# Kernel tuning notes

Measured on AMD Instinct MI355X. Metric: run time of the kernel, lower is better.

Reference implementation:

```python
import jax, jax.numpy as jnp
import numpy as np

N = 100_000      # nodes
E = 1_600_000    # edges (avg degree 16)
H = 2            # heads
C = 32           # out channels per head
L = 4            # EGAT layers
IN = 4           # input one-hot dim (node labels)
ECLS = 5         # edge classes (ratings)
SCALE = 0.1


def setup_inputs() -> dict:
    key = jax.random.key(0)
    ks = jax.random.split(key, 8)
    # node labels arange%4 -> equal user (0) / item (1) counts; x is one-hot (input_embedding=False)
    labels = jnp.arange(N) % 4
    x = jax.nn.one_hot(labels, IN, dtype=jnp.float32)
    edge_index = jax.random.randint(ks[0], (2, E), 0, N)
    edge_attr = jax.random.randint(ks[1], (E,), 0, ECLS)
    W0 = jax.random.normal(ks[2], (IN, H * C), dtype=jnp.float32) * SCALE
    W13 = jax.random.normal(ks[3], (L - 1, H * C, H * C), dtype=jnp.float32) * SCALE
    eemb = jax.random.normal(ks[4], (L, ECLS, H * C), dtype=jnp.float32) * SCALE
    att_src = jax.random.normal(ks[5], (L, H, C), dtype=jnp.float32) * SCALE
    att_dst = jax.random.normal(ks[6], (L, H, C), dtype=jnp.float32) * SCALE
    bias = jnp.zeros((L, H * C), dtype=jnp.float32)
    return dict(x=x, W0=W0, W13=W13, eemb=eemb, att_src=att_src,
                att_dst=att_dst, bias=bias, edge_index=edge_index, edge_attr=edge_attr)


def _egat_layer(x, W, eemb_l, a_src, a_dst, b, src, dst, edge_attr):
    # x: [N, Fin] -> h: [N, H, C]
    h = (x @ W).reshape(N, H, C)
    e = eemb_l[edge_attr].reshape(E, H, C)            # per-edge type embedding
    m = h[src] + e                                    # [E, H, C] edge-featured message
    logits = jax.nn.leaky_relu(
        jnp.sum(h[dst] * a_dst, axis=-1) + jnp.sum(m * a_src, axis=-1), 0.2)  # [E, H]
    # ragged softmax over incoming edges of each destination node
    amax = jax.ops.segment_max(logits, dst, num_segments=N)
    amax = jnp.where(jnp.isfinite(amax), amax, 0.0)
    ex = jnp.exp(logits - amax[dst])
    denom = jax.ops.segment_sum(ex, dst, num_segments=N)
    alpha = ex / (denom[dst] + 1e-16)                 # [E, H]
    out = jax.ops.segment_sum(alpha[..., None] * m, dst, num_segments=N)  # [N, H, C]
    return jax.nn.elu(out.reshape(N, H * C) + b)      # concat heads + elu activation


def reference(x, W0, W13, eemb, att_src, att_dst, bias, edge_index, edge_attr):
    src, dst = edge_index[0], edge_index[1]
    h = _egat_layer(x, W0, eemb[0], att_src[0], att_dst[0], bias[0], src, dst, edge_attr)
    for l in range(1, L):
        h = _egat_layer(h, W13[l - 1], eemb[l], att_src[l], att_dst[l], bias[l], src, dst, edge_attr)
    # users are nodes with label 0 (x[:,0]==1), items label 1 (x[:,1]==1);
    # labels were built as arange(N)%4, so user/item indices are static strided slices.
    user_idx = jnp.arange(0, N, 4)
    item_idx = jnp.arange(1, N, 4)
    u = h[user_idx]
    v = h[item_idx]
    return jnp.sum(u * v, axis=-1)  # MF decoder, multiply_by=1
```

## Files before the change

kernel.cpp:

```cpp
#include <hip/hip_runtime.h>
#include <hip/hip_bf16.h>
#include <math.h>

#define N_NODES 100000
#define N_EDGES 1600000
#define HC 64
#define NHEADS 2
#define NLAYERS 4
#define ECLS 5
#define NBUCK 196
#define NBLK 256
#define EPB (N_EDGES / NBLK)
#define NGRP (N_NODES / 16)
#define LIN0_BLOCKS 1024

typedef __attribute__((ext_vector_type(8))) short short8;
typedef __attribute__((ext_vector_type(4))) float floatx4;
union F8 { uint4 u; short8 s; };

__device__ inline float bf_lo(unsigned int u) { return __uint_as_float(u << 16); }
__device__ inline float bf_hi(unsigned int u) { return __uint_as_float(u & 0xffff0000u); }
__device__ inline unsigned short f2bf(float f) {
    unsigned int u = __float_as_uint(f);
    u += 0x7FFFu + ((u >> 16) & 1u);
    return (unsigned short)(u >> 16);
}

__global__ void k_chist_lin0(const int* __restrict__ dst, int* __restrict__ bh,
                             const float* __restrict__ in,
                             const float* __restrict__ W,
                             const float* __restrict__ asrc, const float* __restrict__ adst,
                             unsigned short* __restrict__ hcurb,
                             float* __restrict__ ssrc, float* __restrict__ sdst) {
    int tid = threadIdx.x;
    if (blockIdx.x < NBLK) {
        __shared__ int lh[NBUCK];
        int blk = blockIdx.x;
        for (int i = tid; i < NBUCK; i += 256) lh[i] = 0;
        __syncthreads();
        int s = blk * EPB, e = s + EPB;
        for (int i = s + tid; i < e; i += 256) atomicAdd(&lh[dst[i] >> 9], 1);
        __syncthreads();
        for (int i = tid; i < NBUCK; i += 256) bh[i * 256 + blk] = lh[i];
        return;
    }
    int j = tid & 63;
    int wid = ((blockIdx.x - NBLK) * 256 + tid) >> 6;
    int nwaves = LIN0_BLOCKS * 4;

    float w0 = W[0 * HC + j], w1 = W[1 * HC + j], w2 = W[2 * HC + j], w3 = W[3 * HC + j];
    int head = j >> 5;
    int c = j & 31;
    float as = asrc[head * 32 + c];
    float ad = adst[head * 32 + c];

    for (int n = wid; n < N_NODES; n += nwaves) {
        int nu = __builtin_amdgcn_readfirstlane(n);
        float4 r = *(const float4*)(in + (size_t)nu * 4);
        float acc = r.x * w0 + r.y * w1 + r.z * w2 + r.w * w3;
        hcurb[(size_t)nu * HC + j] = f2bf(acc);
        float ps = acc * as;
        float pd = acc * ad;
        for (int off = 16; off > 0; off >>= 1) {
            ps += __shfl_down(ps, off, 32);
            pd += __shfl_down(pd, off, 32);
        }
        if (c == 0) {
            ssrc[nu * 2 + head] = ps;
            sdst[nu * 2 + head] = pd;
        }
    }
}

__global__ void k_s1(const int* __restrict__ bh, int* __restrict__ bbase,
                     int* __restrict__ part) {
    __shared__ int tmp[256];
    int tid = threadIdx.x;
    int i = blockIdx.x * 256 + tid;
    int v = bh[i];
    tmp[tid] = v;
    __syncthreads();
    for (int off = 1; off < 256; off <<= 1) {
        int t = (tid >= off) ? tmp[tid - off] : 0;
        __syncthreads();
        tmp[tid] += t;
        __syncthreads();
    }
    bbase[i] = tmp[tid] - v;
    if (tid == 255) part[blockIdx.x] = tmp[255];
}

__global__ void k_s2(int* __restrict__ part,
                     const float* __restrict__ eemb, const float* __restrict__ att_src,
                     float* __restrict__ escore) {
    __shared__ int tmp[256];
    int tid = threadIdx.x;
    int v = (tid < NBUCK) ? part[tid] : 0;
    tmp[tid] = v;
    __syncthreads();
    for (int off = 1; off < 256; off <<= 1) {
        int t = (tid >= off) ? tmp[tid - off] : 0;
        __syncthreads();
        tmp[tid] += t;
        __syncthreads();
    }
    if (tid < NBUCK) part[tid] = tmp[tid] - v;
    if (tid >= 200 && tid < 200 + NLAYERS * ECLS * NHEADS) {
        int idx = tid - 200;
        int l = idx / (ECLS * NHEADS);
        int r = idx % (ECLS * NHEADS);
        int c = r >> 1;
        int h = r & 1;
        float s = 0.f;
        const float* ev = eemb + l * ECLS * HC + c * HC + h * 32;
        const float* av = att_src + l * HC + h * 32;
        for (int k = 0; k < 32; ++k) s += ev[k] * av[k];
        escore[idx] = s;
    }
}

__global__ void k_cscatter(const int* __restrict__ src, const int* __restrict__ dst,
                           const int* __restrict__ attr, const int* __restrict__ bbase,
                           const int* __restrict__ part, int* __restrict__ bkt) {
    __shared__ int cur[NBUCK];
    int tid = threadIdx.x, blk = blockIdx.x;
    for (int i = tid; i < NBUCK; i += 256) cur[i] = bbase[i * 256 + blk] + part[i];
    __syncthreads();
    int s0 = blk * EPB, e0 = s0 + EPB;
    for (int i = s0 + tid; i < e0; i += 256) {
        int d = dst[i];
        int b = d >> 9;
        int pos = atomicAdd(&cur[b], 1);
        bkt[pos] = src[i] | (attr[i] << 17) | ((d & 511) << 20);
    }
}

__global__ void k_fine(const int* __restrict__ part, const int* __restrict__ bkt,
                       int* __restrict__ packed, int* __restrict__ rowstart) {
    __shared__ int hist[512];
    __shared__ int cur[512];
    int b = blockIdx.x, tid = threadIdx.x;
    int base = part[b];
    int bend = (b + 1 < NBUCK) ? part[b + 1] : N_EDGES;
    int nb = bend - base;
    hist[tid] = 0;
    __syncthreads();
    for (int i = tid; i < nb; i += 512)
        atomicAdd(&hist[(bkt[base + i] >> 20) & 0x1FF], 1);
    __syncthreads();
    int v = hist[tid];
    for (int off = 1; off < 512; off <<= 1) {
        int t = (tid >= off) ? hist[tid - off] : 0;
        __syncthreads();
        hist[tid] += t;
        __syncthreads();
    }
    int excl = hist[tid] - v;
    int node = (b << 9) + tid;
    if (node <= N_NODES) rowstart[node] = base + excl;
    cur[tid] = excl;
    __syncthreads();
    for (int i = tid; i < nb; i += 512) {
        int p = bkt[base + i];
        int r = atomicAdd(&cur[(p >> 20) & 0x1FF], 1);
        packed[base + r] = p;
    }
}

__global__ void k_linmfma(const unsigned short* __restrict__ actB,
                          const float* __restrict__ Wl,
                          const float* __restrict__ asrc,
                          const float* __restrict__ adst,
                          unsigned short* __restrict__ hcurb,
                          float* __restrict__ ssrc, float* __restrict__ sdst) {
    __shared__ uint4 WB[512];
    __shared__ unsigned short Cb[4][1024];
    int tid = threadIdx.x;
    int lane = tid & 63;
    int w = tid >> 6;
    int q = lane >> 4;
    int c = lane & 15;

    for (int rid = tid; rid < 512; rid += 256) {
        int kk = rid >> 8;
        int t  = (rid >> 6) & 3;
        int ln = rid & 63;
        int qq = ln >> 4, cc = ln & 15;
        unsigned int u[4];
        #pragma unroll
        for (int jj = 0; jj < 4; ++jj) {
            float v0 = Wl[(kk * 32 + qq * 8 + jj * 2 + 0) * 64 + 16 * t + cc];
            float v1 = Wl[(kk * 32 + qq * 8 + jj * 2 + 1) * 64 + 16 * t + cc];
            u[jj] = (unsigned int)f2bf(v0) | ((unsigned int)f2bf(v1) << 16);
        }
        WB[rid] = make_uint4(u[0], u[1], u[2], u[3]);
    }
    __syncthreads();

    short8 bfr[2][4];
    #pragma unroll
    for (int kk = 0; kk < 2; ++kk)
        #pragma unroll
        for (int t = 0; t < 4; ++t) {
            F8 tmp; tmp.u = WB[(kk * 4 + t) * 64 + lane];
            bfr[kk][t] = tmp.s;
        }

    float as_[4], ad_[4];
    #pragma unroll
    for (int t = 0; t < 4; ++t) {
        as_[t] = asrc[16 * t + c];
        ad_[t] = adst[16 * t + c];
    }

    int wid = (blockIdx.x * 256 + tid) >> 6;
    int nwaves = gridDim.x * 4;

    for (int g = wid; g < NGRP; g += nwaves) {
        int base = g * 16;
        F8 a0, a1;
        a0.u = *(const uint4*)(actB + (size_t)(base + c) * HC + q * 8);
        a1.u = *(const uint4*)(actB + (size_t)(base + c) * HC + 32 + q * 8);

        floatx4 acc[4];
        #pragma unroll
        for (int t = 0; t < 4; ++t) {
            acc[t] = (floatx4){0.f, 0.f, 0.f, 0.f};
            acc[t] = __builtin_amdgcn_mfma_f32_16x16x32_bf16(a0.s, bfr[0][t], acc[t], 0, 0, 0);
            acc[t] = __builtin_amdgcn_mfma_f32_16x16x32_bf16(a1.s, bfr[1][t], acc[t], 0, 0, 0);
        }

        #pragma unroll
        for (int r = 0; r < 4; ++r) {
            float h0s = acc[0][r] * as_[0] + acc[1][r] * as_[1];
            float h1s = acc[2][r] * as_[2] + acc[3][r] * as_[3];
            float h0d = acc[0][r] * ad_[0] + acc[1][r] * ad_[1];
            float h1d = acc[2][r] * ad_[2] + acc[3][r] * ad_[3];
            #pragma unroll
            for (int off = 1; off < 16; off <<= 1) {
                h0s += __shfl_xor(h0s, off, 64);
                h1s += __shfl_xor(h1s, off, 64);
                h0d += __shfl_xor(h0d, off, 64);
                h1d += __shfl_xor(h1d, off, 64);
            }
            if (c == 0) {
                int node = base + q * 4 + r;
                *(float2*)(ssrc + node * 2) = make_float2(h0s, h1s);
                *(float2*)(sdst + node * 2) = make_float2(h0d, h1d);
            }
        }

        #pragma unroll
        for (int t = 0; t < 4; ++t)
            #pragma unroll
            for (int r = 0; r < 4; ++r)
                Cb[w][(q * 4 + r) * 64 + 16 * t + c] = f2bf(acc[t][r]);
        __builtin_amdgcn_wave_barrier();
        const uint4* cf = (const uint4*)&Cb[w][0];
        uint4* gout = (uint4*)(hcurb + (size_t)base * HC);
        gout[lane] = cf[lane];
        gout[64 + lane] = cf[64 + lane];
        __builtin_amdgcn_wave_barrier();
    }
}

template <int NW, bool LAST>
__global__ void k_edge(const int* __restrict__ rowstart, const int* __restrict__ packed,
                       const float* __restrict__ ssrc, const float* __restrict__ sdst,
                       const float* __restrict__ escore_l,
                       const unsigned short* __restrict__ hcurb,
                       const float* __restrict__ eemb_l,
                       const float* __restrict__ bias_l,
                       unsigned short* __restrict__ actnext, float* __restrict__ out) {
    __shared__ float lbuf[NW][64];
    __shared__ float obuf[2][64];
    int w = threadIdx.x >> 6;
    int n = LAST ? (blockIdx.x * 4 + w) : (blockIdx.x * NW + w);
    int lane = threadIdx.x & 63;
    int sub = lane >> 3;
    int q   = lane & 7;
    int h   = q >> 2;

    int beg = rowstart[n];
    int end = rowstart[n + 1];
    float sd = sdst[n * 2 + h];

    float4 a0 = make_float4(0.f, 0.f, 0.f, 0.f);
    float4 a1 = make_float4(0.f, 0.f, 0.f, 0.f);
    float ssum = 0.f;
    for (int i = beg + sub; i < end; i += 8) {
        int p = packed[i];
        int s = p & 0x1FFFF;
        int a = (p >> 17) & 7;
        float lg = sd + ssrc[s * 2 + h] + escore_l[a * 2 + h];
        lg = lg >= 0.f ? lg : 0.2f * lg;
        float wt = __expf(lg);
        uint4 hv = *(const uint4*)(hcurb + (size_t)s * HC + q * 8);
        const float4* ep = (const float4*)(eemb_l + a * HC + q * 8);
        float4 e0 = ep[0], e1 = ep[1];
        a0.x += wt * (bf_lo(hv.x) + e0.x);
        a0.y += wt * (bf_hi(hv.x) + e0.y);
        a0.z += wt * (bf_lo(hv.y) + e0.z);
        a0.w += wt * (bf_hi(hv.y) + e0.w);
        a1.x += wt * (bf_lo(hv.z) + e1.x);
        a1.y += wt * (bf_hi(hv.z) + e1.y);
        a1.z += wt * (bf_lo(hv.w) + e1.z);
        a1.w += wt * (bf_hi(hv.w) + e1.w);
        ssum += wt;
    }
    for (int off = 8; off < 64; off <<= 1) {
        a0.x += __shfl_xor(a0.x, off, 64);
        a0.y += __shfl_xor(a0.y, off, 64);
        a0.z += __shfl_xor(a0.z, off, 64);
        a0.w += __shfl_xor(a0.w, off, 64);
        a1.x += __shfl_xor(a1.x, off, 64);
        a1.y += __shfl_xor(a1.y, off, 64);
        a1.z += __shfl_xor(a1.z, off, 64);
        a1.w += __shfl_xor(a1.w, off, 64);
        ssum  += __shfl_xor(ssum,  off, 64);
    }
    if (sub == 0) {
        ((float4*)&lbuf[w][q * 8])[0] = a0;
        ((float4*)&lbuf[w][q * 8])[1] = a1;
    }
    float ssum_h = __shfl(ssum, (lane >> 5) * 4, 64);
    float inv = 1.f / (ssum_h + 1e-16f);
    __builtin_amdgcn_wave_barrier();
    float v = lbuf[w][lane] * inv + bias_l[lane];
    float o = v > 0.f ? v : (__expf(v) - 1.f);
    if (!LAST) {
        actnext[(size_t)n * HC + lane] = f2bf(o);
    } else {
        obuf[w][lane] = o;
        __syncthreads();
        if (w == 0) {
            float p = obuf[0][lane] * obuf[1][lane];
            for (int off = 32; off > 0; off >>= 1) p += __shfl_down(p, off, 64);
            if (lane == 0) out[blockIdx.x] = p;
        }
    }
}

extern "C" void kernel_launch(void* const* d_in, const int* in_sizes, int n_in,
                              void* d_out, int out_size, void* d_ws, size_t ws_size,
                              hipStream_t stream) {
    const float* x       = (const float*)d_in[0];
    const float* W0      = (const float*)d_in[1];
    const float* W13     = (const float*)d_in[2];
    const float* eemb    = (const float*)d_in[3];
    const float* att_src = (const float*)d_in[4];
    const float* att_dst = (const float*)d_in[5];
    const float* bias    = (const float*)d_in[6];
    const int*   eidx    = (const int*)d_in[7];
    const int*   eattr   = (const int*)d_in[8];
    float* out = (float*)d_out;

    const int* src = eidx;
    const int* dst = eidx + N_EDGES;

    char* wsb = (char*)d_ws;
    size_t off = 0;
    auto alloc = [&](size_t bytes) { char* p = wsb + off; off += (bytes + 255) & ~(size_t)255; return p; };
    unsigned short* hcurb  = (unsigned short*)alloc((size_t)N_NODES * HC * 2);
    unsigned short* actB   = (unsigned short*)alloc((size_t)N_NODES * HC * 2);
    float*          ssrc   = (float*)alloc((size_t)N_NODES * 2 * 4);
    float*          sdst   = (float*)alloc((size_t)N_NODES * 2 * 4);
    float*          escore = (float*)alloc(NLAYERS * ECLS * NHEADS * 4);
    int*            bh     = (int*)alloc((size_t)NBUCK * 256 * 4);
    int*            bbase  = (int*)alloc((size_t)NBUCK * 256 * 4);
    int*            part   = (int*)alloc(256 * 4);
    int*            rowstart = (int*)alloc(((size_t)N_NODES + 1) * 4);
    int*            bkt    = (int*)alloc((size_t)N_EDGES * 4);
    int*            packed = (int*)alloc((size_t)N_EDGES * 4);

    k_chist_lin0<<<NBLK + LIN0_BLOCKS, 256, 0, stream>>>(
        dst, bh, x, W0, att_src, att_dst, hcurb, ssrc, sdst);
    k_s1<<<NBUCK, 256, 0, stream>>>(bh, bbase, part);
    k_s2<<<1, 256, 0, stream>>>(part, eemb, att_src, escore);
    k_cscatter<<<NBLK, 256, 0, stream>>>(src, dst, eattr, bbase, part, bkt);
    k_fine<<<NBUCK, 512, 0, stream>>>(part, bkt, packed, rowstart);

    for (int l = 0; l < NLAYERS; ++l) {
        if (l > 0) {
            k_linmfma<<<512, 256, 0, stream>>>(
                actB, W13 + (size_t)(l - 1) * HC * HC,
                att_src + l * HC, att_dst + l * HC, hcurb, ssrc, sdst);
        }
        const float* esl = escore + l * ECLS * NHEADS;
        const float* el  = eemb + (size_t)l * ECLS * HC;
        const float* bl  = bias + l * HC;
        if (l < NLAYERS - 1)
            k_edge<1, false><<<N_NODES, 64, 0, stream>>>(
                rowstart, packed, ssrc, sdst, esl, hcurb, el, bl, actB, nullptr);
        else
            k_edge<2, true><<<N_NODES / 4, 128, 0, stream>>>(
                rowstart, packed, ssrc, sdst, esl, hcurb, el, bl, nullptr, out);
    }
}
```

Before: 341.4 us.

## Stage bucket scatters in shared memory for coalesced writes, double scatter blocks

The coarse scatter now builds a local histogram and prefix per block, sorts its edges into shared memory by bucket, and then writes them out contiguously, so global stores are coalesced rather than random. The fine sort likewise stages each bucket in shared memory (up to a 12288-entry cap) before a linear write-out. The number of scatter blocks is doubled so each block's edge chunk fits in LDS. This costs an extra histogram pass and a lot of shared memory per block, which may reduce occupancy.

Result: faster. 333.4 us (-2.3%).

```diff
diff --git a/kernel.cpp b/kernel.cpp
--- a/kernel.cpp
+++ b/kernel.cpp
@@ -9,10 +9,11 @@
 #define NLAYERS 4
 #define ECLS 5
 #define NBUCK 196
-#define NBLK 256
+#define NBLK 512
 #define EPB (N_EDGES / NBLK)
 #define NGRP (N_NODES / 16)
 #define LIN0_BLOCKS 1024
+#define FCAP 12288
 
 typedef __attribute__((ext_vector_type(8))) short short8;
 typedef __attribute__((ext_vector_type(4))) float floatx4;
@@ -38,10 +39,10 @@
         int blk = blockIdx.x;
         for (int i = tid; i < NBUCK; i += 256) lh[i] = 0;
         __syncthreads();
-        int s = blk * EPB, e = s + EPB;
-        for (int i = s + tid; i < e; i += 256) atomicAdd(&lh[dst[i] >> 9], 1);
-        __syncthreads();
-        for (int i = tid; i < NBUCK; i += 256) bh[i * 256 + blk] = lh[i];
+        int s = blk * EPB;
+        for (int i = tid; i < EPB; i += 256) atomicAdd(&lh[dst[s + i] >> 9], 1);
+        __syncthreads();
+        for (int i = tid; i < NBUCK; i += 256) bh[i * NBLK + blk] = lh[i];
         return;
     }
     int j = tid & 63;
@@ -74,20 +75,20 @@
 
 __global__ void k_s1(const int* __restrict__ bh, int* __restrict__ bbase,
                      int* __restrict__ part) {
-    __shared__ int tmp[256];
+    __shared__ int tmp[NBLK];
     int tid = threadIdx.x;
-    int i = blockIdx.x * 256 + tid;
+    int i = blockIdx.x * NBLK + tid;
     int v = bh[i];
     tmp[tid] = v;
     __syncthreads();
-    for (int off = 1; off < 256; off <<= 1) {
+    for (int off = 1; off < NBLK; off <<= 1) {
         int t = (tid >= off) ? tmp[tid - off] : 0;
         __syncthreads();
         tmp[tid] += t;
         __syncthreads();
     }
     bbase[i] = tmp[tid] - v;
-    if (tid == 255) part[blockIdx.x] = tmp[255];
+    if (tid == NBLK - 1) part[blockIdx.x] = tmp[NBLK - 1];
 }
 
 __global__ void k_s2(int* __restrict__ part,
@@ -122,23 +123,50 @@
 __global__ void k_cscatter(const int* __restrict__ src, const int* __restrict__ dst,
                            const int* __restrict__ attr, const int* __restrict__ bbase,
                            const int* __restrict__ part, int* __restrict__ bkt) {
+    __shared__ int tmp[256];
     __shared__ int cur[NBUCK];
+    __shared__ int gadj[NBUCK];
+    __shared__ int stage[EPB];
+    __shared__ unsigned char stb[EPB];
     int tid = threadIdx.x, blk = blockIdx.x;
-    for (int i = tid; i < NBUCK; i += 256) cur[i] = bbase[i * 256 + blk] + part[i];
-    __syncthreads();
-    int s0 = blk * EPB, e0 = s0 + EPB;
-    for (int i = s0 + tid; i < e0; i += 256) {
-        int d = dst[i];
+    for (int i = tid; i < NBUCK; i += 256) cur[i] = 0;
+    __syncthreads();
+    int s0 = blk * EPB;
+    for (int i = tid; i < EPB; i += 256) atomicAdd(&cur[dst[s0 + i] >> 9], 1);
+    __syncthreads();
+    int v = (tid < NBUCK) ? cur[tid] : 0;
+    tmp[tid] = v;
+    __syncthreads();
+    for (int off = 1; off < 256; off <<= 1) {
+        int t = (tid >= off) ? tmp[tid - off] : 0;
+        __syncthreads();
+        tmp[tid] += t;
+        __syncthreads();
+    }
+    int ex = tmp[tid] - v;
+    if (tid < NBUCK) {
+        cur[tid] = ex;
+        gadj[tid] = bbase[tid * NBLK + blk] + part[tid] - ex;
+    }
+    __syncthreads();
+    for (int i = tid; i < EPB; i += 256) {
+        int e = s0 + i;
+        int d = dst[e];
         int b = d >> 9;
         int pos = atomicAdd(&cur[b], 1);
-        bkt[pos] = src[i] | (attr[i] << 17) | ((d & 511) << 20);
-    }
+        stage[pos] = src[e] | (attr[e] << 17) | ((d & 511) << 20);
+        stb[pos] = (unsigned char)b;
+    }
+    __syncthreads();
+    for (int i = tid; i < EPB; i += 256)
+        bkt[gadj[stb[i]] + i] = stage[i];
 }
 
 __global__ void k_fine(const int* __restrict__ part, const int* __restrict__ bkt,
                        int* __restrict__ packed, int* __restrict__ rowstart) {
     __shared__ int hist[512];
     __shared__ int cur[512];
+    __shared__ int stage[FCAP];
     int b = blockIdx.x, tid = threadIdx.x;
     int base = part[b];
     int bend = (b + 1 < NBUCK) ? part[b + 1] : N_EDGES;
@@ -160,10 +188,20 @@
     if (node <= N_NODES) rowstart[node] = base + excl;
     cur[tid] = excl;
     __syncthreads();
-    for (int i = tid; i < nb; i += 512) {
-        int p = bkt[base + i];
-        int r = atomicAdd(&cur[(p >> 20) & 0x1FF], 1);
-        packed[base + r] = p;
+    if (nb <= FCAP) {
+        for (int i = tid; i < nb; i += 512) {
+            int p = bkt[base + i];
+            int r = atomicAdd(&cur[(p >> 20) & 0x1FF], 1);
+            stage[r] = p;
+        }
+        __syncthreads();
+        for (int i = tid; i < nb; i += 512) packed[base + i] = stage[i];
+    } else {
+        for (int i = tid; i < nb; i += 512) {
+            int p = bkt[base + i];
+            int r = atomicAdd(&cur[(p >> 20) & 0x1FF], 1);
+            packed[base + r] = p;
+        }
     }
 }
 
@@ -366,8 +404,8 @@
     float*          ssrc   = (float*)alloc((size_t)N_NODES * 2 * 4);
     float*          sdst   = (float*)alloc((size_t)N_NODES * 2 * 4);
     float*          escore = (float*)alloc(NLAYERS * ECLS * NHEADS * 4);
-    int*            bh     = (int*)alloc((size_t)NBUCK * 256 * 4);
-    int*            bbase  = (int*)alloc((size_t)NBUCK * 256 * 4);
+    int*            bh     = (int*)alloc((size_t)NBUCK * NBLK * 4);
+    int*            bbase  = (int*)alloc((size_t)NBUCK * NBLK * 4);
     int*            part   = (int*)alloc(256 * 4);
     int*            rowstart = (int*)alloc(((size_t)N_NODES + 1) * 4);
     int*            bkt    = (int*)alloc((size_t)N_EDGES * 4);
@@ -375,7 +413,7 @@
 
     k_chist_lin0<<<NBLK + LIN0_BLOCKS, 256, 0, stream>>>(
         dst, bh, x, W0, att_src, att_dst, hcurb, ssrc, sdst);
-    k_s1<<<NBUCK, 256, 0, stream>>>(bh, bbase, part);
+    k_s1<<<NBUCK, NBLK, 0, stream>>>(bh, bbase, part);
     k_s2<<<1, 256, 0, stream>>>(part, eemb, att_src, escore);
     k_cscatter<<<NBLK, 256, 0, stream>>>(src, dst, eattr, bbase, part, bkt);
     k_fine<<<NBUCK, 512, 0, stream>>>(part, bkt, packed, rowstart);
```
